# Kernel optimization log

Measured on AMD Instinct MI355X. Metric: run time of the kernel, lower is better.

The kernel has to match this reference:

```python
import jax, jax.numpy as jnp
import numpy as np

EPS = 1e-5

def layer_norm(x, g, b):
    mu = jnp.mean(x, axis=-1, keepdims=True)
    var = jnp.mean(jnp.square(x - mu), axis=-1, keepdims=True)
    return (x - mu) * jax.lax.rsqrt(var + EPS) * g + b

def setup_inputs() -> dict:
    key = jax.random.key(0)
    B, N, IN_D, S, D = 64, 4096, 256, 8, 256
    ks = jax.random.split(key, 20)
    scale = lambda fan_in: 1.0 / np.sqrt(fan_in)
    u = lambda k, shape, s: jax.random.uniform(k, shape, jnp.float32, -s, s)
    return {
        "inputs": jax.random.normal(ks[0], (B, N, IN_D), jnp.float32),
        "noise": jax.random.normal(ks[1], (B, S, D), jnp.float32),
        "slots_mu": jax.random.normal(ks[2], (1, S, D), jnp.float32),
        "slots_sigma": jnp.ones((1, S, D), jnp.float32) * 0.1,
        "Wq": u(ks[3], (D, D), scale(D)), "bq": u(ks[4], (D,), scale(D)),
        "Wk": u(ks[5], (D, IN_D), scale(IN_D)), "bk": u(ks[6], (D,), scale(IN_D)),
        "Wv": u(ks[7], (D, IN_D), scale(IN_D)), "bv": u(ks[8], (D,), scale(IN_D)),
        "W_ih": u(ks[9], (3 * D, D), scale(D)), "b_ih": u(ks[10], (3 * D,), scale(D)),
        "W_hh": u(ks[11], (3 * D, D), scale(D)), "b_hh": u(ks[12], (3 * D,), scale(D)),
        "W1": u(ks[13], (D, D), scale(D)), "b1": u(ks[14], (D,), scale(D)),
        "W2": u(ks[15], (D, D), scale(D)), "b2": u(ks[16], (D,), scale(D)),
        "ln_slots_g": jnp.ones((D,), jnp.float32), "ln_slots_b": jnp.zeros((D,), jnp.float32),
        "ln_mlp_g": jnp.ones((D,), jnp.float32), "ln_mlp_b": jnp.zeros((D,), jnp.float32),
    }

def gru_cell(x, h, W_ih, b_ih, W_hh, b_hh):
    # PyTorch GRUCell: gates ordered (reset, update, new)
    gi = x @ W_ih.T + b_ih  # [B*S, 3D]
    gh = h @ W_hh.T + b_hh
    i_r, i_z, i_n = jnp.split(gi, 3, axis=-1)
    h_r, h_z, h_n = jnp.split(gh, 3, axis=-1)
    r = jax.nn.sigmoid(i_r + h_r)
    z = jax.nn.sigmoid(i_z + h_z)
    n = jnp.tanh(i_n + r * h_n)
    return (1.0 - z) * n + z * h

def reference(inputs, noise, slots_mu, slots_sigma, Wq, bq, Wk, bk, Wv, bv,
              W_ih, b_ih, W_hh, b_hh, W1, b1, W2, b2,
              ln_slots_g, ln_slots_b, ln_mlp_g, ln_mlp_b):
    B, N, _ = inputs.shape
    _, S, D = noise.shape
    num_iterations = 3
    slots = slots_mu + slots_sigma * noise  # [B, S, D]
    # k, v are loop-invariant; hoist the big GEMMs out of the iteration loop
    k = jnp.einsum('bnd,ed->bne', inputs, Wk) + bk  # [B, N, D]
    v = jnp.einsum('bnd,ed->bne', inputs, Wv) + bv  # [B, N, D]
    inv_sqrt_d = 1.0 / np.sqrt(D)
    for _ in range(num_iterations):
        slots_prev = slots
        q = layer_norm(slots, ln_slots_g, ln_slots_b) @ Wq.T + bq  # [B, S, D]
        attn_logits = jnp.einsum('bsd,bnd->bsn', q, k) * inv_sqrt_d
        attn = jax.nn.softmax(attn_logits, axis=-1)  # softmax over inputs (dim=-1)
        updates = jnp.einsum('bsn,bnd->bsd', attn, v)  # [B, S, D]
        h_new = gru_cell(updates.reshape(-1, D), slots_prev.reshape(-1, D),
                         W_ih, b_ih, W_hh, b_hh).reshape(B, S, D)
        slots = slots_prev + h_new  # residual around GRU (as in source)
        hidden = jax.nn.relu(layer_norm(slots, ln_mlp_g, ln_mlp_b) @ W1.T + b1)
        slots = slots + (hidden @ W2.T + b2)
    return slots
```

## Files before the change

### kernel.cpp

```cpp
#include <hip/hip_runtime.h>


constexpr int Bn = 64;
constexpr int Nn = 4096;
constexpr int Dd = 256;
constexpr int Ss = 8;
constexpr int CH = 16;
constexpr float EPSF = 1e-5f;

#define DEV __device__ __forceinline__

using short8 = __attribute__((ext_vector_type(8))) short;
using f32x4 = __attribute__((ext_vector_type(4))) float;
union U8 { short8 s; uint4 u; };

DEV unsigned bfpack2(float lo, float hi) {
  unsigned ul = __float_as_uint(lo), uh = __float_as_uint(hi);
  ul = (ul + 0x7FFFu + ((ul >> 16) & 1u)) >> 16;
  uh = (uh + 0x7FFFu + ((uh >> 16) & 1u)) & 0xFFFF0000u;
  return ul | uh;
}
DEV unsigned short bf16r(float x) {
  unsigned u = __float_as_uint(x);
  u = (u + 0x7FFFu + ((u >> 16) & 1u)) >> 16;
  return (unsigned short)u;
}
DEV float rsum32(float v) {
  v += __shfl_xor(v, 1); v += __shfl_xor(v, 2); v += __shfl_xor(v, 4);
  v += __shfl_xor(v, 8); v += __shfl_xor(v, 16);
  return v;
}
DEV float sigm(float x) { return 1.f / (1.f + __expf(-x)); }

template <int NK>
DEV void load_af(short8* a, const unsigned short* base, int lda, int m16, int quad) {
  const unsigned short* p = base + m16 * lda + quad * 8;
#pragma unroll
  for (int kk = 0; kk < NK; ++kk) a[kk] = *(const short8*)(p + kk * 32);
}
template <int NK>
DEV f32x4 gemm_tile(const short8* a, const unsigned short* wr, float binit) {
  f32x4 acc = {binit, binit, binit, binit};
#pragma unroll
  for (int kk = 0; kk < NK; ++kk) {
    short8 b = *(const short8*)(wr + kk * 32);
    acc = __builtin_amdgcn_mfma_f32_16x16x32_bf16(a[kk], b, acc, 0, 0, 0);
  }
  return acc;
}

DEV void ln_row8(const float* x, const float* g, const float* b, int d0,
                 unsigned short* dst) {
  float s = x[0] + x[1] + x[2] + x[3] + x[4] + x[5] + x[6] + x[7];
  float mu = rsum32(s) * (1.f / 256.f);
  float q = 0.f;
#pragma unroll
  for (int j = 0; j < 8; ++j) { float d = x[j] - mu; q += d * d; }
  float rs = rsqrtf(rsum32(q) * (1.f / 256.f) + EPSF);
  float o[8];
#pragma unroll
  for (int j = 0; j < 8; ++j) o[j] = (x[j] - mu) * rs * g[d0 + j] + b[d0 + j];
  uint4 w;
  w.x = bfpack2(o[0], o[1]); w.y = bfpack2(o[2], o[3]);
  w.z = bfpack2(o[4], o[5]); w.w = bfpack2(o[6], o[7]);
  *(uint4*)dst = w;
}

__global__ __launch_bounds__(256) void k_wqk(const float* __restrict__ Wq,
                                             const float* __restrict__ Wk,
                                             const float* __restrict__ bq,
                                             unsigned short* __restrict__ Wqk_b,
                                             float* __restrict__ bqk) {
  int tid = threadIdx.x, c = blockIdx.x;
  if (c < 256) {
    float acc = 0.f;
    for (int e = 0; e < 256; ++e) acc += Wq[e * 256 + tid] * Wk[e * 256 + c];
    Wqk_b[c * 256 + tid] = bf16r(acc);
  } else {
    float acc = 0.f;
    for (int e = 0; e < 256; ++e) acc += bq[e] * Wk[e * 256 + tid];
    bqk[tid] = acc;
  }
}

__global__ __launch_bounds__(256) void k_conv(
    const float* __restrict__ Wv, const float* __restrict__ Wih,
    const float* __restrict__ Whh, const float* __restrict__ W1,
    const float* __restrict__ W2,
    const float* __restrict__ bih, const float* __restrict__ bhh,
    unsigned* Wv_b, unsigned* Wzr_b, unsigned* Win_b, unsigned* Whn_b,
    unsigned* W1_b, unsigned* W2_b, float* bzr) {
  if (blockIdx.x >= 1152) {
    int i = (blockIdx.x - 1152) * 256 + threadIdx.x;
    if (i < 512) bzr[i] = bih[i] + bhh[i];
    return;
  }
  int p = blockIdx.x * 256 + threadIdx.x;
  const float* src; unsigned* dst;
  if (p < 32768) { src = Wv + 2 * p; dst = Wv_b + p; }
  else if (p < 163840) {
    int q = p - 32768, row = q >> 8, col = (q & 255) * 2;
    src = (col < 256) ? (Wih + row * 256 + col) : (Whh + row * 256 + col - 256);
    dst = Wzr_b + q;
  }
  else if (p < 196608) { int q = p - 163840; src = Wih + 512 * 256 + 2 * q; dst = Win_b + q; }
  else if (p < 229376) { int q = p - 196608; src = Whh + 512 * 256 + 2 * q; dst = Whn_b + q; }
  else if (p < 262144) { int q = p - 229376; src = W1 + 2 * q; dst = W1_b + q; }
  else { int q = p - 262144; src = W2 + 2 * q; dst = W2_b + q; }
  dst[0] = bfpack2(src[0], src[1]);
}

__global__ __launch_bounds__(512) void k_qk0(const float* __restrict__ noise,
                                             const float* __restrict__ s_mu,
                                             const float* __restrict__ s_sg,
                                             const float* __restrict__ gsl,
                                             const float* __restrict__ bsl,
                                             const unsigned short* __restrict__ Wqk_b,
                                             const float* __restrict__ bqk,
                                             float* __restrict__ slots,
                                             float* __restrict__ qk) {
  __shared__ __align__(16) unsigned short lnb[16 * 264];
  const int tid = threadIdx.x, bb = blockIdx.x;
  const int lane = tid & 63, wave = tid >> 6;
  const int m16 = lane & 15, quad = lane >> 4;
  const int row = tid >> 5, l32 = tid & 31, d0 = l32 * 8;
  {
    const int grow = bb * 16 + row;
    const int sidx = (grow & 7) * 256 + d0;
    const float* np = noise + (size_t)grow * 256 + d0;
    float4 n0 = *(const float4*)np, n1 = *(const float4*)(np + 4);
    float4 m0 = *(const float4*)(s_mu + sidx), m1 = *(const float4*)(s_mu + sidx + 4);
    float4 g0 = *(const float4*)(s_sg + sidx), g1 = *(const float4*)(s_sg + sidx + 4);
    float x[8] = {m0.x + g0.x * n0.x, m0.y + g0.y * n0.y,
                  m0.z + g0.z * n0.z, m0.w + g0.w * n0.w,
                  m1.x + g1.x * n1.x, m1.y + g1.y * n1.y,
                  m1.z + g1.z * n1.z, m1.w + g1.w * n1.w};
    float* sp_ = slots + (size_t)grow * 256 + d0;
    float4 o0, o1;
    o0.x = x[0]; o0.y = x[1]; o0.z = x[2]; o0.w = x[3];
    o1.x = x[4]; o1.y = x[5]; o1.z = x[6]; o1.w = x[7];
    *(float4*)sp_ = o0; *(float4*)(sp_ + 4) = o1;
    ln_row8(x, gsl, bsl, d0, lnb + row * 264 + d0);
  }
  __syncthreads();
  short8 a8[8];
  load_af<8>(a8, lnb, 264, m16, quad);
#pragma unroll
  for (int i = 0; i < 2; ++i) {
    int t = wave + 8 * i;
    f32x4 acc = gemm_tile<8>(a8, Wqk_b + (size_t)(t * 16 + m16) * 256 + quad * 8,
                             bqk[t * 16 + m16]);
#pragma unroll
    for (int r = 0; r < 4; ++r)
      qk[(size_t)(bb * 16 + quad * 4 + r) * 256 + t * 16 + m16] = acc[r] * 0.0625f;
  }
}

template <bool FIRST>
DEV void ld_chunk(const float* __restrict__ xin, unsigned* __restrict__ xbf,
                  size_t nbase, int tid, uint4* pr) {
#pragma unroll
  for (int i = 0; i < 4; ++i) {
    int flat = i * 256 + tid, n = flat >> 5, od = flat & 31;
    if (FIRST) {
      const float4* src = (const float4*)(xin + (nbase + n) * 256 + od * 8);
      float4 v0 = src[0], v1 = src[1];
      uint4 o;
      o.x = bfpack2(v0.x, v0.y); o.y = bfpack2(v0.z, v0.w);
      o.z = bfpack2(v1.x, v1.y); o.w = bfpack2(v1.z, v1.w);
      ((uint4*)xbf)[(nbase + n) * 32 + od] = o;
      pr[i] = o;
    } else {
      pr[i] = ((const uint4*)xbf)[(nbase + n) * 32 + od];
    }
  }
}

template <bool FIRST>
__global__ __launch_bounds__(256) void k_attn(const float* __restrict__ xin,
                                              unsigned* __restrict__ xbf,
                                              const float* __restrict__ qk,
                                              float* __restrict__ pl,
                                              float* __restrict__ pu) {
  __shared__ __align__(16) unsigned xt[2][128 * 33];
  __shared__ __align__(16) unsigned pp[2][16 * 17];
  __shared__ __align__(16) float lred[2][16];
  const int tid = threadIdx.x;
  const int lane = tid & 63, wave = tid >> 6;
  const int m16 = lane & 15, quad = lane >> 4;
  const int c = blockIdx.x, b = blockIdx.y;
  const int pb = (b * CH + c) * 8;
  const bool isA = (wave < 2);
  const unsigned psel = (m16 & 1) ? 0x07060302u : 0x05040100u;

  short8 aq[8];
  if (isA) {
    const float* qrow = qk + (size_t)(b * 8 + (m16 & 7)) * 256 + quad * 8;
#pragma unroll
    for (int kk = 0; kk < 8; ++kk) {
      U8 f;
      float4 q0 = *(const float4*)(qrow + kk * 32);
      float4 q1 = *(const float4*)(qrow + kk * 32 + 4);
      f.u.x = bfpack2(q0.x, q0.y); f.u.y = bfpack2(q0.z, q0.w);
      f.u.z = bfpack2(q1.x, q1.y); f.u.w = bfpack2(q1.z, q1.w);
      if (m16 >= 8) { f.u.x = 0u; f.u.y = 0u; f.u.z = 0u; f.u.w = 0u; }
      aq[kk] = f.s;
    }
  }
  float lacc[4] = {0.f, 0.f, 0.f, 0.f};
  f32x4 acc[8];
#pragma unroll
  for (int t = 0; t < 8; ++t) acc[t] = (f32x4){0.f, 0.f, 0.f, 0.f};

  uint4 pr[4];
  const size_t nb0 = (size_t)b * Nn + (size_t)c * 256;
  ld_chunk<FIRST>(xin, xbf, nb0, tid, pr);

  for (int ch = 0; ch <= 8; ++ch) {
    if (ch < 8) {
      unsigned* xtb = xt[ch & 1];
#pragma unroll
      for (int i = 0; i < 4; ++i) {
        int flat = i * 256 + tid, n = flat >> 5, od = flat & 31, rb = od * 4;
        xtb[(rb + 0) * 33 + n] = pr[i].x;
        xtb[(rb + 1) * 33 + n] = pr[i].y;
        xtb[(rb + 2) * 33 + n] = pr[i].z;
        xtb[(rb + 3) * 33 + n] = pr[i].w;
      }
    }
    __syncthreads();
    if (ch + 1 < 8)
      ld_chunk<FIRST>(xin, xbf, nb0 + (size_t)(ch + 1) * 32, tid, pr);
    if (isA) {
      if (ch < 8) {
        const unsigned* xtb = xt[ch & 1];
        f32x4 pacc = (f32x4){0.f, 0.f, 0.f, 0.f};
#pragma unroll
        for (int kk = 0; kk < 8; ++kk) {
          int base = (kk * 16 + quad * 4) * 33 + wave * 16 + m16;
          U8 bf;
          bf.u.x = xtb[base]; bf.u.y = xtb[base + 33];
          bf.u.z = xtb[base + 66]; bf.u.w = xtb[base + 99];
          pacc = __builtin_amdgcn_mfma_f32_16x16x32_bf16(aq[kk], bf.s, pacc, 0, 0, 0);
        }
        const int xrow = wave * 16 + m16;
        unsigned short* pps = (unsigned short*)pp[ch & 1];
#pragma unroll
        for (int r = 0; r < 4; ++r) {
          float p = __expf(pacc[r]);
          lacc[r] += p;
          pps[((xrow >> 1) * 17 + quad * 4 + r) * 2 + (xrow & 1)] = bf16r(p);
        }
      }
    } else if (ch >= 1) {
      const unsigned* xtb = xt[(ch - 1) & 1];
      const unsigned* ppb = pp[(ch - 1) & 1];
      U8 bp;
      bp.u.x = ppb[(quad * 4 + 0) * 17 + m16];
      bp.u.y = ppb[(quad * 4 + 1) * 17 + m16];
      bp.u.z = ppb[(quad * 4 + 2) * 17 + m16];
      bp.u.w = ppb[(quad * 4 + 3) * 17 + m16];
#pragma unroll
      for (int t = 0; t < 8; ++t) {
        int d = (wave - 2) * 128 + t * 16 + m16;
        const unsigned* xr = xtb + (d >> 1) * 33 + quad * 8;
        unsigned u0 = xr[0], u1 = xr[1], u2 = xr[2], u3 = xr[3];
        unsigned u4 = xr[4], u5 = xr[5], u6 = xr[6], u7 = xr[7];
        U8 af;
        af.u.x = __builtin_amdgcn_perm(u1, u0, psel);
        af.u.y = __builtin_amdgcn_perm(u3, u2, psel);
        af.u.z = __builtin_amdgcn_perm(u5, u4, psel);
        af.u.w = __builtin_amdgcn_perm(u7, u6, psel);
        acc[t] = __builtin_amdgcn_mfma_f32_16x16x32_bf16(af.s, bp.s, acc[t], 0, 0, 0);
      }
    }
    __syncthreads();
  }
  if (!isA && m16 < 8) {
    const int d0w = (wave - 2) * 128;
#pragma unroll
    for (int t = 0; t < 8; ++t)
#pragma unroll
      for (int r = 0; r < 4; ++r)
        pu[(size_t)(pb + m16) * 256 + d0w + t * 16 + quad * 4 + r] = acc[t][r];
  }
  if (isA) {
#pragma unroll
    for (int r = 0; r < 4; ++r) {
      float v = lacc[r];
      v += __shfl_xor(v, 1); v += __shfl_xor(v, 2);
      v += __shfl_xor(v, 4); v += __shfl_xor(v, 8);
      if (m16 == 0) lred[wave][quad * 4 + r] = v;
    }
  }
  __syncthreads();
  if (tid < 8) pl[pb + tid] = lred[0][tid] + lred[1][tid];
}

__global__ __launch_bounds__(512) void k_upd(
    const float* __restrict__ pl, const float* __restrict__ pu,
    const unsigned short* __restrict__ Wv_b, const float* __restrict__ bv,
    const unsigned short* __restrict__ Wzr_b, const float* __restrict__ bzr,
    const unsigned short* __restrict__ Win_b, const float* __restrict__ bin,
    const unsigned short* __restrict__ Whn_b, const float* __restrict__ bhn,
    const unsigned short* __restrict__ W1_b, const float* __restrict__ b1,
    const unsigned short* __restrict__ W2_b, const float* __restrict__ b2,
    const float* __restrict__ gml, const float* __restrict__ bml,
    const float* __restrict__ gsl, const float* __restrict__ bsl,
    const unsigned short* __restrict__ Wqk_b, const float* __restrict__ bqk,
    float* __restrict__ slots, float* __restrict__ qk, float* __restrict__ dout) {
  __shared__ __align__(16) unsigned short cat[16 * 520];
  __shared__ __align__(16) float sp[16 * 260];
  __shared__ __align__(16) float s1[16 * 260];
  __shared__ __align__(16) unsigned short lnb[16 * 264];
  const int tid = threadIdx.x, bb = blockIdx.x;
  const int lane = tid & 63, wave = tid >> 6;
  const int m16 = lane & 15, quad = lane >> 4;
  const int row = tid >> 5, l32 = tid & 31, d0 = l32 * 8;
  const int bat = 2 * bb + (row >> 3), sl = row & 7;
  {
    float L = 0.f;
#pragma unroll
    for (int cc = 0; cc < 16; ++cc) L += pl[(bat * 16 + cc) * 8 + sl];
    float li = 1.f / L;
    float a[8] = {0.f, 0.f, 0.f, 0.f, 0.f, 0.f, 0.f, 0.f};
    for (int cc = 0; cc < 16; ++cc) {
      const float* pp_ = pu + ((size_t)(bat * 16 + cc) * 8 + sl) * 256 + d0;
      float4 v0 = *(const float4*)pp_, v1 = *(const float4*)(pp_ + 4);
      a[0] += v0.x; a[1] += v0.y; a[2] += v0.z; a[3] += v0.w;
      a[4] += v1.x; a[5] += v1.y; a[6] += v1.z; a[7] += v1.w;
    }
    uint4 o;
    o.x = bfpack2(a[0] * li, a[1] * li); o.y = bfpack2(a[2] * li, a[3] * li);
    o.z = bfpack2(a[4] * li, a[5] * li); o.w = bfpack2(a[6] * li, a[7] * li);
    *(uint4*)(cat + row * 520 + d0) = o;
    const float* sp_ = slots + (size_t)(bb * 16 + row) * 256 + d0;
    float4 h0 = *(const float4*)sp_, h1 = *(const float4*)(sp_ + 4);
    *(float4*)(sp + row * 260 + d0) = h0;
    *(float4*)(sp + row * 260 + d0 + 4) = h1;
    uint4 hb;
    hb.x = bfpack2(h0.x, h0.y); hb.y = bfpack2(h0.z, h0.w);
    hb.z = bfpack2(h1.x, h1.y); hb.w = bfpack2(h1.z, h1.w);
    *(uint4*)(cat + row * 520 + 256 + d0) = hb;
  }
  __syncthreads();
  short8 afr[16];
  load_af<8>(afr, cat, 520, m16, quad);
  f32x4 accv[2];
#pragma unroll
  for (int i = 0; i < 2; ++i) {
    int t = wave + 8 * i;
    accv[i] = gemm_tile<8>(afr, Wv_b + (size_t)(t * 16 + m16) * 256 + quad * 8,
                           bv[t * 16 + m16]);
  }
  __syncthreads();
#pragma unroll
  for (int i = 0; i < 2; ++i) {
    int t = wave + 8 * i;
#pragma unroll
    for (int r = 0; r < 4; ++r)
      cat[(quad * 4 + r) * 520 + t * 16 + m16] = bf16r(accv[i][r]);
  }
  __syncthreads();
  load_af<16>(afr, cat, 520, m16, quad);
  f32x4 rr[2], zz[2];
#pragma unroll
  for (int i = 0; i < 2; ++i) {
    int t = wave + 8 * i;
    f32x4 ar = gemm_tile<16>(afr, Wzr_b + (size_t)(t * 16 + m16) * 512 + quad * 8,
                             bzr[t * 16 + m16]);
    f32x4 az = gemm_tile<16>(afr, Wzr_b + (size_t)((t + 16) * 16 + m16) * 512 + quad * 8,
                             bzr[(t + 16) * 16 + m16]);
#pragma unroll
    for (int r = 0; r < 4; ++r) { rr[i][r] = sigm(ar[r]); zz[i][r] = sigm(az[r]); }
  }
#pragma unroll
  for (int i = 0; i < 2; ++i) {
    int t = wave + 8 * i, col = t * 16 + m16;
    f32x4 ain = gemm_tile<8>(afr, Win_b + (size_t)(t * 16 + m16) * 256 + quad * 8,
                             bin[col]);
    f32x4 ahn = gemm_tile<8>(afr + 8, Whn_b + (size_t)(t * 16 + m16) * 256 + quad * 8,
                             bhn[col]);
#pragma unroll
    for (int r = 0; r < 4; ++r) {
      int rw = quad * 4 + r;
      float nin = ain[r] + rr[i][r] * ahn[r];
      float nn = 1.f - 2.f / (__expf(2.f * nin) + 1.f);
      float hpc = sp[rw * 260 + col];
      s1[rw * 260 + col] = hpc + (1.f - zz[i][r]) * nn + zz[i][r] * hpc;
    }
  }
  __syncthreads();
  {
    const float* s1r = s1 + row * 260 + d0;
    float4 v0 = *(const float4*)s1r, v1 = *(const float4*)(s1r + 4);
    float x[8] = {v0.x, v0.y, v0.z, v0.w, v1.x, v1.y, v1.z, v1.w};
    ln_row8(x, gml, bml, d0, lnb + row * 264 + d0);
  }
  __syncthreads();
  load_af<8>(afr, lnb, 264, m16, quad);
#pragma unroll
  for (int i = 0; i < 2; ++i) {
    int t = wave + 8 * i;
    f32x4 acc = gemm_tile<8>(afr, W1_b + (size_t)(t * 16 + m16) * 256 + quad * 8,
                             b1[t * 16 + m16]);
#pragma unroll
    for (int r = 0; r < 4; ++r)
      cat[(quad * 4 + r) * 520 + t * 16 + m16] = bf16r(fmaxf(acc[r], 0.f));
  }
  __syncthreads();
  load_af<8>(afr, cat, 520, m16, quad);
#pragma unroll
  for (int i = 0; i < 2; ++i) {
    int t = wave + 8 * i;
    f32x4 acc = gemm_tile<8>(afr, W2_b + (size_t)(t * 16 + m16) * 256 + quad * 8,
                             b2[t * 16 + m16]);
#pragma unroll
    for (int r = 0; r < 4; ++r) {
      int rw = quad * 4 + r, col = t * 16 + m16;
      float v = acc[r] + s1[rw * 260 + col];
      size_t gi = (size_t)(bb * 16 + rw) * 256 + col;
      slots[gi] = v;
      if (dout) dout[gi] = v;
      sp[rw * 260 + col] = v;
    }
  }
  __syncthreads();
  {
    const float* spr = sp + row * 260 + d0;
    float4 v0 = *(const float4*)spr, v1 = *(const float4*)(spr + 4);
    float x[8] = {v0.x, v0.y, v0.z, v0.w, v1.x, v1.y, v1.z, v1.w};
    ln_row8(x, gsl, bsl, d0, lnb + row * 264 + d0);
  }
  __syncthreads();
  load_af<8>(afr, lnb, 264, m16, quad);
#pragma unroll
  for (int i = 0; i < 2; ++i) {
    int t = wave + 8 * i;
    f32x4 acc = gemm_tile<8>(afr, Wqk_b + (size_t)(t * 16 + m16) * 256 + quad * 8,
                             bqk[t * 16 + m16]);
#pragma unroll
    for (int r = 0; r < 4; ++r)
      qk[(size_t)(bb * 16 + quad * 4 + r) * 256 + t * 16 + m16] = acc[r] * 0.0625f;
  }
}

extern "C" void kernel_launch(void* const* d_in, const int* in_sizes, int n_in,
                              void* d_out, int out_size, void* d_ws, size_t ws_size,
                              hipStream_t stream) {
  const float* inputs = (const float*)d_in[0];
  const float* noise = (const float*)d_in[1];
  const float* s_mu = (const float*)d_in[2];
  const float* s_sg = (const float*)d_in[3];
  const float* Wq = (const float*)d_in[4];
  const float* bq = (const float*)d_in[5];
  const float* Wk = (const float*)d_in[6];
  const float* Wv = (const float*)d_in[8];
  const float* bv = (const float*)d_in[9];
  const float* Wih = (const float*)d_in[10];
  const float* bih = (const float*)d_in[11];
  const float* Whh = (const float*)d_in[12];
  const float* bhh = (const float*)d_in[13];
  const float* W1 = (const float*)d_in[14];
  const float* b1 = (const float*)d_in[15];
  const float* W2 = (const float*)d_in[16];
  const float* b2 = (const float*)d_in[17];
  const float* gsl = (const float*)d_in[18];
  const float* bsl = (const float*)d_in[19];
  const float* gml = (const float*)d_in[20];
  const float* bml = (const float*)d_in[21];
  float* out = (float*)d_out;

  char* wsb = (char*)d_ws;
  unsigned* xbf = (unsigned*)wsb;
  float* fp = (float*)(wsb + (size_t)Bn * Nn * Dd * 2);
  float* slots = fp; fp += Bn * Ss * Dd;
  float* qk = fp;    fp += Bn * Ss * Dd;
  float* bqk = fp;   fp += Dd;
  float* pl = fp;    fp += Bn * CH * Ss;
  float* pu = fp;    fp += Bn * CH * Ss * Dd;
  float* bzr = fp;   fp += 512;
  unsigned short* wb = (unsigned short*)fp;
  unsigned short* Wv_b = wb;  wb += 65536;
  unsigned short* Wzr_b = wb; wb += 262144;
  unsigned short* Win_b = wb; wb += 65536;
  unsigned short* Whn_b = wb; wb += 65536;
  unsigned short* W1_b = wb;  wb += 65536;
  unsigned short* W2_b = wb;  wb += 65536;
  unsigned short* Wqk_b = wb; wb += 65536;
  (void)in_sizes; (void)n_in; (void)out_size; (void)ws_size;

  k_wqk<<<dim3(257), dim3(256), 0, stream>>>(Wq, Wk, bq, Wqk_b, bqk);
  k_conv<<<dim3(1154), dim3(256), 0, stream>>>(
      Wv, Wih, Whh, W1, W2, bih, bhh, (unsigned*)Wv_b, (unsigned*)Wzr_b,
      (unsigned*)Win_b, (unsigned*)Whn_b, (unsigned*)W1_b, (unsigned*)W2_b, bzr);
  k_qk0<<<dim3(32), dim3(512), 0, stream>>>(noise, s_mu, s_sg, gsl, bsl, Wqk_b, bqk,
                                            slots, qk);
  for (int it = 0; it < 3; ++it) {
    if (it == 0)
      k_attn<true><<<dim3(CH, Bn), dim3(256), 0, stream>>>(inputs, xbf, qk, pl, pu);
    else
      k_attn<false><<<dim3(CH, Bn), dim3(256), 0, stream>>>(nullptr, xbf, qk, pl, pu);
    k_upd<<<dim3(32), dim3(512), 0, stream>>>(
        pl, pu, Wv_b, bv, Wzr_b, bzr, Win_b, bih + 512, Whn_b, bhh + 512, W1_b, b1,
        W2_b, b2, gml, bml, gsl, bsl, Wqk_b, bqk, slots, qk, (it == 2) ? out : nullptr);
  }
}
```

Measured before the change: 679.6 us.

## Replace wave-specialized attention pipeline with uniform waves over 64-row chunks

The attention kernel previously split its four waves into two that computed logits/exp and two that accumulated the value product one chunk behind, using double-buffered shared memory over eight 32-row chunks. Now every wave computes one 16-row logits tile and then accumulates a 64-column slice of the value product, over four 64-row chunks with a single buffer and two barriers per chunk. This is meant to remove the idle imbalance between producer and consumer waves and halve the loop trip count. In exchange it loses the overlap between the two stages, doubles the register prefetch buffer, and needs more barriers per chunk.

```diff
diff --git a/kernel.cpp b/kernel.cpp
--- a/kernel.cpp
+++ b/kernel.cpp
@@ -160,7 +160,7 @@
 DEV void ld_chunk(const float* __restrict__ xin, unsigned* __restrict__ xbf,
                   size_t nbase, int tid, uint4* pr) {
 #pragma unroll
-  for (int i = 0; i < 4; ++i) {
+  for (int i = 0; i < 8; ++i) {
     int flat = i * 256 + tid, n = flat >> 5, od = flat & 31;
     if (FIRST) {
       const float4* src = (const float4*)(xin + (nbase + n) * 256 + od * 8);
@@ -182,19 +182,18 @@
                                               const float* __restrict__ qk,
                                               float* __restrict__ pl,
                                               float* __restrict__ pu) {
-  __shared__ __align__(16) unsigned xt[2][128 * 33];
-  __shared__ __align__(16) unsigned pp[2][16 * 17];
-  __shared__ __align__(16) float lred[2][16];
+  __shared__ __align__(16) unsigned xt[128 * 65];
+  __shared__ __align__(16) unsigned pp[32 * 17];
+  __shared__ __align__(16) float lred[4][16];
   const int tid = threadIdx.x;
   const int lane = tid & 63, wave = tid >> 6;
   const int m16 = lane & 15, quad = lane >> 4;
   const int c = blockIdx.x, b = blockIdx.y;
   const int pb = (b * CH + c) * 8;
-  const bool isA = (wave < 2);
   const unsigned psel = (m16 & 1) ? 0x07060302u : 0x05040100u;
 
   short8 aq[8];
-  if (isA) {
+  {
     const float* qrow = qk + (size_t)(b * 8 + (m16 & 7)) * 256 + quad * 8;
 #pragma unroll
     for (int kk = 0; kk < 8; ++kk) {
@@ -208,62 +207,59 @@
     }
   }
   float lacc[4] = {0.f, 0.f, 0.f, 0.f};
-  f32x4 acc[8];
-#pragma unroll
-  for (int t = 0; t < 8; ++t) acc[t] = (f32x4){0.f, 0.f, 0.f, 0.f};
-
-  uint4 pr[4];
+  f32x4 acc[4];
+#pragma unroll
+  for (int t = 0; t < 4; ++t) acc[t] = (f32x4){0.f, 0.f, 0.f, 0.f};
+  const int d0w = wave * 64;
+
+  uint4 pr[8];
   const size_t nb0 = (size_t)b * Nn + (size_t)c * 256;
   ld_chunk<FIRST>(xin, xbf, nb0, tid, pr);
 
-  for (int ch = 0; ch <= 8; ++ch) {
-    if (ch < 8) {
-      unsigned* xtb = xt[ch & 1];
-#pragma unroll
-      for (int i = 0; i < 4; ++i) {
-        int flat = i * 256 + tid, n = flat >> 5, od = flat & 31, rb = od * 4;
-        xtb[(rb + 0) * 33 + n] = pr[i].x;
-        xtb[(rb + 1) * 33 + n] = pr[i].y;
-        xtb[(rb + 2) * 33 + n] = pr[i].z;
-        xtb[(rb + 3) * 33 + n] = pr[i].w;
+  for (int ch = 0; ch < 4; ++ch) {
+#pragma unroll
+    for (int i = 0; i < 8; ++i) {
+      int flat = i * 256 + tid, n = flat >> 5, od = flat & 31, rb = od * 4;
+      xt[(rb + 0) * 65 + n] = pr[i].x;
+      xt[(rb + 1) * 65 + n] = pr[i].y;
+      xt[(rb + 2) * 65 + n] = pr[i].z;
+      xt[(rb + 3) * 65 + n] = pr[i].w;
+    }
+    __syncthreads();
+    if (ch + 1 < 4)
+      ld_chunk<FIRST>(xin, xbf, nb0 + (size_t)(ch + 1) * 64, tid, pr);
+    {
+      const int nt = wave;
+      f32x4 pacc = (f32x4){0.f, 0.f, 0.f, 0.f};
+#pragma unroll
+      for (int kk = 0; kk < 8; ++kk) {
+        int base = (kk * 16 + quad * 4) * 65 + nt * 16 + m16;
+        U8 bf;
+        bf.u.x = xt[base]; bf.u.y = xt[base + 65];
+        bf.u.z = xt[base + 130]; bf.u.w = xt[base + 195];
+        pacc = __builtin_amdgcn_mfma_f32_16x16x32_bf16(aq[kk], bf.s, pacc, 0, 0, 0);
       }
+      const int xrow = nt * 16 + m16;
+      unsigned short* pps = (unsigned short*)pp;
+#pragma unroll
+      for (int r = 0; r < 4; ++r) {
+        float p = __expf(pacc[r]);
+        lacc[r] += p;
+        pps[((xrow >> 1) * 17 + quad * 4 + r) * 2 + (xrow & 1)] = bf16r(p);
+      }
     }
     __syncthreads();
-    if (ch + 1 < 8)
-      ld_chunk<FIRST>(xin, xbf, nb0 + (size_t)(ch + 1) * 32, tid, pr);
-    if (isA) {
-      if (ch < 8) {
-        const unsigned* xtb = xt[ch & 1];
-        f32x4 pacc = (f32x4){0.f, 0.f, 0.f, 0.f};
-#pragma unroll
-        for (int kk = 0; kk < 8; ++kk) {
-          int base = (kk * 16 + quad * 4) * 33 + wave * 16 + m16;
-          U8 bf;
-          bf.u.x = xtb[base]; bf.u.y = xtb[base + 33];
-          bf.u.z = xtb[base + 66]; bf.u.w = xtb[base + 99];
-          pacc = __builtin_amdgcn_mfma_f32_16x16x32_bf16(aq[kk], bf.s, pacc, 0, 0, 0);
-        }
-        const int xrow = wave * 16 + m16;
-        unsigned short* pps = (unsigned short*)pp[ch & 1];
-#pragma unroll
-        for (int r = 0; r < 4; ++r) {
-          float p = __expf(pacc[r]);
-          lacc[r] += p;
-          pps[((xrow >> 1) * 17 + quad * 4 + r) * 2 + (xrow & 1)] = bf16r(p);
-        }
-      }
-    } else if (ch >= 1) {
-      const unsigned* xtb = xt[(ch - 1) & 1];
-      const unsigned* ppb = pp[(ch - 1) & 1];
+#pragma unroll
+    for (int nh = 0; nh < 2; ++nh) {
       U8 bp;
-      bp.u.x = ppb[(quad * 4 + 0) * 17 + m16];
-      bp.u.y = ppb[(quad * 4 + 1) * 17 + m16];
-      bp.u.z = ppb[(quad * 4 + 2) * 17 + m16];
-      bp.u.w = ppb[(quad * 4 + 3) * 17 + m16];
-#pragma unroll
-      for (int t = 0; t < 8; ++t) {
-        int d = (wave - 2) * 128 + t * 16 + m16;
-        const unsigned* xr = xtb + (d >> 1) * 33 + quad * 8;
+      bp.u.x = pp[(nh * 16 + quad * 4 + 0) * 17 + m16];
+      bp.u.y = pp[(nh * 16 + quad * 4 + 1) * 17 + m16];
+      bp.u.z = pp[(nh * 16 + quad * 4 + 2) * 17 + m16];
+      bp.u.w = pp[(nh * 16 + quad * 4 + 3) * 17 + m16];
+#pragma unroll
+      for (int t = 0; t < 4; ++t) {
+        int d = d0w + t * 16 + m16;
+        const unsigned* xr = xt + (d >> 1) * 65 + nh * 32 + quad * 8;
         unsigned u0 = xr[0], u1 = xr[1], u2 = xr[2], u3 = xr[3];
         unsigned u4 = xr[4], u5 = xr[5], u6 = xr[6], u7 = xr[7];
         U8 af;
@@ -276,15 +272,14 @@
     }
     __syncthreads();
   }
-  if (!isA && m16 < 8) {
-    const int d0w = (wave - 2) * 128;
-#pragma unroll
-    for (int t = 0; t < 8; ++t)
+  if (m16 < 8) {
+#pragma unroll
+    for (int t = 0; t < 4; ++t)
 #pragma unroll
       for (int r = 0; r < 4; ++r)
         pu[(size_t)(pb + m16) * 256 + d0w + t * 16 + quad * 4 + r] = acc[t][r];
   }
-  if (isA) {
+  {
 #pragma unroll
     for (int r = 0; r < 4; ++r) {
       float v = lacc[r];
@@ -294,7 +289,8 @@
     }
   }
   __syncthreads();
-  if (tid < 8) pl[pb + tid] = lred[0][tid] + lred[1][tid];
+  if (tid < 8)
+    pl[pb + tid] = lred[0][tid] + lred[1][tid] + lred[2][tid] + lred[3][tid];
 }
 
 __global__ __launch_bounds__(512) void k_upd(
```

Result: no change. 686.5 us (+1.0%).
